# Performance work log

Measured on AMD Instinct MI355X. Metric: run time of the kernel, lower is better.

The kernel has to match this reference:

```python
import jax, jax.numpy as jnp
import numpy as np

NUM_HEADS = 16
ROPE_BASE = 50.0


def _apply_rope(x):
    # x: [b, s, h, d]; torchtune-style rotary embedding with base=ROPE_BASE
    b, s, h, d = x.shape
    inv_freq = 1.0 / (ROPE_BASE ** (jnp.arange(0, d, 2, dtype=jnp.float32) / d))  # [d/2]
    angles = jnp.arange(s, dtype=jnp.float32)[:, None] * inv_freq[None, :]         # [s, d/2]
    cos = jnp.cos(angles)[None, :, None, :]  # [1, s, 1, d/2]
    sin = jnp.sin(angles)[None, :, None, :]
    xr = x.reshape(b, s, h, d // 2, 2)
    x0, x1 = xr[..., 0], xr[..., 1]
    out = jnp.stack([x0 * cos - x1 * sin, x1 * cos + x0 * sin], axis=-1)
    return out.reshape(b, s, h, d).astype(x.dtype)


def setup_inputs() -> dict:
    key = jax.random.key(0)
    k1, k2, k3 = jax.random.split(key, 3)
    B, S, D = 2, 2048, 1024
    x = jax.random.normal(k1, (B, S, D), dtype=jnp.float32)
    w_qkv = jax.random.normal(k2, (3 * D, D), dtype=jnp.float32) * (D ** -0.5)
    w_out = jax.random.normal(k3, (D, D), dtype=jnp.float32) * (D ** -0.5)
    b_out = jnp.zeros((D,), dtype=jnp.float32)
    return {"x": x, "w_qkv": w_qkv, "w_out": w_out, "b_out": b_out}


def reference(x, w_qkv, w_out, b_out):
    B, S, D = x.shape
    H = NUM_HEADS
    dk = D // H

    qkv = x @ w_qkv.T                       # [b, s, 3D]
    q, k, v = jnp.split(qkv, 3, axis=-1)
    q = q.reshape(B, S, H, dk)
    k = k.reshape(B, S, H, dk)
    q = _apply_rope(q)
    k = _apply_rope(k)
    q = q.transpose(0, 2, 1, 3)             # [b, h, s, d]
    k = k.transpose(0, 2, 1, 3)
    v = v.reshape(B, S, H, dk).transpose(0, 2, 1, 3)

    scale = 1.0 / jnp.sqrt(jnp.asarray(dk, dtype=x.dtype))
    scores = jnp.einsum('bhsd,bhtd->bhst', q, k) * scale  # [b, h, s, s]
    # additive diagonal mask: -inf on the diagonal (blocks self-attention)
    eye = jnp.eye(S, dtype=bool)
    scores = jnp.where(eye[None, None], -jnp.inf, scores)
    attn = jax.nn.softmax(scores, axis=-1)
    out = jnp.einsum('bhst,bhtd->bhsd', attn, v)          # [b, h, s, d]
    out = out.transpose(0, 2, 1, 3).reshape(B, S, D)
    return out @ w_out.T + b_out
```

## Files before the change

kernel.cpp:

```cpp
#include <hip/hip_runtime.h>
#include <hip/hip_bf16.h>
#include <math.h>

#define D_MODEL 1024
#define NHEADS  16
#define DK      64
#define SEQ     2048
#define BATCH   2
#define QTILE   128

typedef __attribute__((ext_vector_type(8)))  short  short8;
typedef __attribute__((ext_vector_type(8)))  unsigned short ushort8;
typedef __attribute__((ext_vector_type(4)))  float  floatx4;
typedef __attribute__((ext_vector_type(16))) float  floatx16;

__device__ __forceinline__ unsigned short f2bf(float f) {
    union { float f; unsigned int u; } v; v.f = f;
    unsigned int u = v.u;
    return (unsigned short)((u + 0x7FFFu + ((u >> 16) & 1u)) >> 16);
}
__device__ __forceinline__ float bf2f(unsigned short u) {
    union { unsigned int u; float f; } v; v.u = ((unsigned int)u) << 16;
    return v.f;
}
__device__ __forceinline__ unsigned int fau(float f) {
    union { float f; unsigned int u; } v; v.f = f; return v.u;
}

__device__ __forceinline__ void gload_lds16(const unsigned short* g, unsigned short* l) {
    __builtin_amdgcn_global_load_lds((__attribute__((address_space(1))) const void*)g,
                                     (__attribute__((address_space(3))) void*)l,
                                     16, 0, 0);
}

#define X8 ((BATCH * SEQ * D_MODEL) / 8)
#define W8 ((3 * D_MODEL * D_MODEL) / 8)
#define O8 ((D_MODEL * D_MODEL) / 8)
__global__ __launch_bounds__(256) void pack_all(const float* __restrict__ x,
                                                const float* __restrict__ wq,
                                                const float* __restrict__ wo,
                                                unsigned short* __restrict__ xb,
                                                unsigned short* __restrict__ wqb,
                                                unsigned short* __restrict__ wob) {
    const int t = blockIdx.x * blockDim.x + threadIdx.x;
    const float* src; unsigned short* dst; int idx;
    if (t < X8)           { src = x;  dst = xb;  idx = t; }
    else if (t < X8 + W8) { src = wq; dst = wqb; idx = t - X8; }
    else if (t < X8 + W8 + O8) { src = wo; dst = wob; idx = t - X8 - W8; }
    else return;
    const float4 a = ((const float4*)src)[2 * idx];
    const float4 b = ((const float4*)src)[2 * idx + 1];
    short8 o;
    o[0] = (short)f2bf(a.x); o[1] = (short)f2bf(a.y);
    o[2] = (short)f2bf(a.z); o[3] = (short)f2bf(a.w);
    o[4] = (short)f2bf(b.x); o[5] = (short)f2bf(b.y);
    o[6] = (short)f2bf(b.z); o[7] = (short)f2bf(b.w);
    ((short8*)dst)[idx] = o;
}

template <int TM, typename OUT_T>
__global__ __launch_bounds__(256) void gemm_bf16(const unsigned short* __restrict__ A,
                                                 const unsigned short* __restrict__ B,
                                                 const float* __restrict__ bias,
                                                 OUT_T* __restrict__ C,
                                                 int M, int N, int K) {
    constexpr int NAF = TM / 32;
    __shared__ __align__(16) unsigned short As[TM][32];
    __shared__ __align__(16) unsigned short Bs[128][32];

    const int tid  = threadIdx.x;
    const int wave = tid >> 6;
    const int lane = tid & 63;
    const int quad = lane >> 4;
    const int lcol = lane & 15;
    const int wr   = (wave >> 1) * (TM / 2);
    const int wc   = (wave & 1) * 64;
    const int tm   = blockIdx.y * TM;
    const int tn   = blockIdx.x * 128;

    const int srowA = wave * (TM / 4) + (lane >> 2);
    const int srowB = wave * 32 + (lane >> 2);
    const int scol  = (lane & 3) * 8;
    const unsigned short* gB0 = B + (size_t)(tn + srowB) * K + scol;
    const unsigned short* gB1 = gB0 + (size_t)16 * K;
    unsigned short* lB0 = &Bs[wave * 32][0];
    unsigned short* lB1 = &Bs[wave * 32 + 16][0];

    floatx4 acc[NAF][4];
#pragma unroll
    for (int i = 0; i < NAF; ++i)
#pragma unroll
        for (int j = 0; j < 4; ++j) acc[i][j] = (floatx4){0.f, 0.f, 0.f, 0.f};

    for (int k0 = 0; k0 < K; k0 += 32) {
        __syncthreads();
#pragma unroll
        for (int u = 0; u < TM / 64; ++u)
            gload_lds16(A + (size_t)(tm + srowA + u * 16) * K + k0 + scol,
                        &As[wave * (TM / 4) + u * 16][0]);
        gload_lds16(gB0 + k0, lB0);
        gload_lds16(gB1 + k0, lB1);
        __syncthreads();

        short8 af[NAF], bf[4];
#pragma unroll
        for (int i = 0; i < NAF; ++i) af[i] = *(short8*)&As[wr + i * 16 + lcol][quad * 8];
#pragma unroll
        for (int j = 0; j < 4; ++j) bf[j] = *(short8*)&Bs[wc + j * 16 + lcol][quad * 8];
#pragma unroll
        for (int i = 0; i < NAF; ++i)
#pragma unroll
            for (int j = 0; j < 4; ++j)
                acc[i][j] = __builtin_amdgcn_mfma_f32_16x16x32_bf16(af[i], bf[j], acc[i][j], 0, 0, 0);
    }

#pragma unroll
    for (int i = 0; i < NAF; ++i) {
#pragma unroll
        for (int r = 0; r < 4; ++r) {
            const int row = tm + wr + i * 16 + quad * 4 + r;
#pragma unroll
            for (int j = 0; j < 4; ++j) {
                const int col = tn + wc + j * 16 + lcol;
                float v = acc[i][j][r];
                if (bias) v += bias[col];
                if constexpr (sizeof(OUT_T) == 2)
                    C[(size_t)row * N + col] = (OUT_T)f2bf(v);
                else
                    C[(size_t)row * N + col] = (OUT_T)v;
            }
        }
    }
}

__global__ __launch_bounds__(256) void rope_vtrans(const unsigned short* __restrict__ qkvb,
                                                   unsigned short* __restrict__ Qb,
                                                   unsigned short* __restrict__ Kb,
                                                   unsigned short* __restrict__ Vtg) {
    const int st = blockIdx.x, h = blockIdx.y, b = blockIdx.z;
    const int tid = threadIdx.x;
    const int s0 = st * 64;

    const int i  = tid & 31;
    const int r0 = tid >> 5;
    const float inv_freq = exp2f(-(2.0f * (float)i / (float)DK) * log2f(50.0f));
    const float QSCALE = 0.125f * 1.44269504f;
#pragma unroll
    for (int pass = 0; pass < 8; ++pass) {
        const int s = s0 + r0 + pass * 8;
        const size_t in_base = ((size_t)(b * SEQ + s)) * (3 * D_MODEL) + h * DK + 2 * i;
        const float q0 = bf2f(qkvb[in_base]),           q1 = bf2f(qkvb[in_base + 1]);
        const float k0 = bf2f(qkvb[in_base + D_MODEL]), k1 = bf2f(qkvb[in_base + D_MODEL + 1]);
        float sn, cs;
        __sincosf((float)s * inv_freq, &sn, &cs);
        const size_t ob = (((size_t)(b * NHEADS + h)) * SEQ + s) * DK + 2 * i;
        const unsigned int qw = (unsigned int)f2bf((q0 * cs - q1 * sn) * QSCALE)
                              | ((unsigned int)f2bf((q1 * cs + q0 * sn) * QSCALE) << 16);
        const unsigned int kw = (unsigned int)f2bf(k0 * cs - k1 * sn)
                              | ((unsigned int)f2bf(k1 * cs + k0 * sn) << 16);
        *(unsigned int*)&Qb[ob] = qw;
        *(unsigned int*)&Kb[ob] = kw;
    }

    __shared__ unsigned short Lt[64][65];
    const int r = tid >> 3;
    const int c = (tid & 7) * 8;
    const size_t in_row = ((size_t)(b * SEQ + s0 + r)) * (3 * D_MODEL) + 2 * D_MODEL + h * DK + c;
    const ushort8 v0 = *(const ushort8*)&qkvb[in_row];
    const ushort8 v1 = *(const ushort8*)&qkvb[in_row + (size_t)32 * (3 * D_MODEL)];
    const int u0 = r, u1 = r + 32;
    const int kc0 = (u0 & 48) | (8 * ((u0 >> 2) & 1) + (u0 & 3) + 4 * ((u0 >> 3) & 1));
    const int kc1 = (u1 & 48) | (8 * ((u1 >> 2) & 1) + (u1 & 3) + 4 * ((u1 >> 3) & 1));
#pragma unroll
    for (int j = 0; j < 8; ++j) Lt[c + j][kc0] = v0[j];
#pragma unroll
    for (int j = 0; j < 8; ++j) Lt[c + j][kc1] = v1[j];
    __syncthreads();
    const size_t bh = (size_t)(b * NHEADS + h);
    ushort8 o0, o1;
#pragma unroll
    for (int j = 0; j < 8; ++j) { o0[j] = Lt[r][c + j]; o1[j] = Lt[r + 32][c + j]; }
    unsigned short* orow = Vtg + (bh * DK + r) * SEQ + s0 + c;
    *(ushort8*)orow = o0;
    *(ushort8*)(orow + (size_t)32 * SEQ) = o1;
}

#define LDW 72

__global__ __launch_bounds__(512, 4) void flash_attn(const unsigned short* __restrict__ Qb,
                                                     const unsigned short* __restrict__ Kb,
                                                     const unsigned short* __restrict__ Vtg,
                                                     unsigned short* __restrict__ attnb) {
    const int tid  = threadIdx.x;
    const int wave = tid >> 6;
    const int lane = tid & 63;
    const int l31  = lane & 31;
    const int lh   = lane >> 5;
    const int mh2  = wave & 3;
    const int kh   = wave >> 2;
    const int kb   = kh * 32;

    const int f  = blockIdx.x + gridDim.x * (blockIdx.y + gridDim.y * blockIdx.z);
    const int w  = (f & 7) * 64 + (f >> 3);
    const int qt = w & 15;
    const int h  = (w >> 4) & 15;
    const int b  = w >> 8;

    __shared__ __align__(16) unsigned char smem[36864];
    unsigned short (*Ks0)[LDW] = (unsigned short (*)[LDW])(smem);
    unsigned short (*Vt0)[LDW] = (unsigned short (*)[LDW])(smem +  9216);
    unsigned short (*Ks1)[LDW] = (unsigned short (*)[LDW])(smem + 18432);
    unsigned short (*Vt1)[LDW] = (unsigned short (*)[LDW])(smem + 27648);
    float (*Ored)[68] = (float (*)[68])smem;
    float* lred0 = (float*)(smem + 34816);
    float* lred1 = lred0 + 128;

    const size_t bh = (size_t)(b * NHEADS + h);
    const unsigned short* Qg = Qb + (bh * SEQ + (size_t)qt * QTILE) * DK;
    const unsigned short* Kg = Kb + bh * SEQ * DK;
    const unsigned short* Vg = Vtg + bh * (size_t)DK * SEQ;

    short8 qf[4];
#pragma unroll
    for (int t = 0; t < 4; ++t)
        qf[t] = *(const short8*)&Qg[(size_t)(mh2 * 32 + l31) * DK + t * 16 + lh * 8];

    const int strow = tid >> 3;
    const int stcol = (tid & 7) * 8;
    const unsigned short* kg = &Kg[(size_t)strow * DK + stcol];
    const unsigned short* vg = &Vg[(size_t)strow * SEQ + stcol];

    short8 kr = *(const short8*)&kg[0];
    short8 vr = *(const short8*)&vg[0];

    floatx16 oacc[2];
    oacc[0] = (floatx16)(0.f);
    oacc[1] = (floatx16)(0.f);
    float lp = 0.f;

    const int diagkt = qt * QTILE + mh2 * 32 - kb;

    auto compute = [&](unsigned short (*Ks)[LDW], unsigned short (*Vt)[LDW], int kt) {
        floatx16 sc = (floatx16)(0.f);
        __builtin_amdgcn_s_setprio(1);
#pragma unroll
        for (int t = 0; t < 4; ++t) {
            const short8 kf = *(short8*)&Ks[kb + l31][t * 16 + lh * 8];
            sc = __builtin_amdgcn_mfma_f32_32x32x16_bf16(kf, qf[t], sc, 0, 0, 0);
        }
        __builtin_amdgcn_s_setprio(0);

        if (kt == diagkt) {
#pragma unroll
            for (int r = 0; r < 16; ++r) {
                const int key_loc = (r & 3) + 8 * (r >> 2) + 4 * lh;
                if (key_loc == l31) sc[r] = -1e30f;
            }
        }

        short8 pf0, pf1;
        {
            union { unsigned int u[4]; short8 s8; } a, c;
#pragma unroll
            for (int d = 0; d < 4; ++d) {
                const float e0 = __builtin_amdgcn_exp2f(sc[2 * d]);
                const float e1 = __builtin_amdgcn_exp2f(sc[2 * d + 1]);
                a.u[d] = __builtin_amdgcn_perm(fau(e1), fau(e0), 0x07060302u);
                const float f0 = __builtin_amdgcn_exp2f(sc[8 + 2 * d]);
                const float f1 = __builtin_amdgcn_exp2f(sc[8 + 2 * d + 1]);
                c.u[d] = __builtin_amdgcn_perm(fau(f1), fau(f0), 0x07060302u);
                lp += (e0 + e1) + (f0 + f1);
            }
            pf0 = a.s8;
            pf1 = c.s8;
        }

        __builtin_amdgcn_s_setprio(1);
#pragma unroll
        for (int nd = 0; nd < 2; ++nd) {
            const short8 vfa = *(short8*)&Vt[nd * 32 + l31][kb + lh * 8];
            const short8 vfb = *(short8*)&Vt[nd * 32 + l31][kb + 16 + lh * 8];
            oacc[nd] = __builtin_amdgcn_mfma_f32_32x32x16_bf16(pf0, vfa, oacc[nd], 0, 0, 0);
            oacc[nd] = __builtin_amdgcn_mfma_f32_32x32x16_bf16(pf1, vfb, oacc[nd], 0, 0, 0);
        }
        __builtin_amdgcn_s_setprio(0);
    };

    for (int kt = 0; kt < SEQ; kt += 128) {
        *(short8*)&Ks0[strow][stcol] = kr;
        *(short8*)&Vt0[strow][stcol] = vr;
        __syncthreads();
        kr = *(const short8*)&kg[(size_t)(kt + 64) * DK];
        vr = *(const short8*)&vg[kt + 64];
        compute(Ks0, Vt0, kt);

        *(short8*)&Ks1[strow][stcol] = kr;
        *(short8*)&Vt1[strow][stcol] = vr;
        __syncthreads();
        const int ktn = (kt + 128 < SEQ) ? kt + 128 : 0;
        kr = *(const short8*)&kg[(size_t)ktn * DK];
        vr = *(const short8*)&vg[ktn];
        compute(Ks1, Vt1, kt + 64);
    }

    const float lptot = lp + __shfl_xor(lp, 32, 64);

    __syncthreads();
    if (lh == 0) {
        if (kh == 0) lred0[mh2 * 32 + l31] = lptot;
        else         lred1[mh2 * 32 + l31] = lptot;
    }
    if (kh == 1) {
#pragma unroll
        for (int r = 0; r < 16; ++r) {
            const int m = mh2 * 32 + (r & 3) + 8 * (r >> 2) + 4 * lh;
            Ored[m][l31]      = oacc[0][r];
            Ored[m][32 + l31] = oacc[1][r];
        }
    }
    __syncthreads();
    if (kh == 0) {
        unsigned short* obase = attnb + ((size_t)b * SEQ + (size_t)qt * QTILE) * D_MODEL + h * DK;
#pragma unroll
        for (int r = 0; r < 16; ++r) {
            const int m = mh2 * 32 + (r & 3) + 8 * (r >> 2) + 4 * lh;
            const float inv = 1.001953125f / (lred0[m] + lred1[m]);
            const float v0 = (oacc[0][r] + Ored[m][l31]) * inv;
            const float v1 = (oacc[1][r] + Ored[m][32 + l31]) * inv;
            obase[(size_t)m * D_MODEL + l31]      = f2bf(v0);
            obase[(size_t)m * D_MODEL + 32 + l31] = f2bf(v1);
        }
    }
}

extern "C" void kernel_launch(void* const* d_in, const int* in_sizes, int n_in,
                              void* d_out, int out_size, void* d_ws, size_t ws_size,
                              hipStream_t stream) {
    const float* x     = (const float*)d_in[0];
    const float* w_qkv = (const float*)d_in[1];
    const float* w_out = (const float*)d_in[2];
    const float* b_out = (const float*)d_in[3];
    float* out = (float*)d_out;

    const int M = BATCH * SEQ;
    const size_t X_ELEMS    = (size_t)M * D_MODEL;
    const size_t WQKV_ELEMS = (size_t)3 * D_MODEL * D_MODEL;
    const size_t WOUT_ELEMS = (size_t)D_MODEL * D_MODEL;
    const size_t QKV_ELEMS  = (size_t)M * 3 * D_MODEL;
    const size_t HEAD_ELEMS = (size_t)BATCH * NHEADS * SEQ * DK;

    unsigned short* xb    = (unsigned short*)d_ws;
    unsigned short* wqkvb = xb + X_ELEMS;
    unsigned short* woutb = wqkvb + WQKV_ELEMS;
    unsigned short* qkvb  = woutb + WOUT_ELEMS;
    unsigned short* Qb    = qkvb + QKV_ELEMS;
    unsigned short* Kb    = Qb + HEAD_ELEMS;
    unsigned short* Vtg   = Kb + HEAD_ELEMS;
    unsigned short* attnb = Vtg + HEAD_ELEMS;

    pack_all<<<(X8 + W8 + O8 + 255) / 256, 256, 0, stream>>>(x, w_qkv, w_out, xb, wqkvb, woutb);

    {
        dim3 grid(3 * D_MODEL / 128, M / 128);
        gemm_bf16<128, unsigned short><<<grid, 256, 0, stream>>>(xb, wqkvb, nullptr, qkvb,
                                                                 M, 3 * D_MODEL, D_MODEL);
    }
    {
        dim3 grid(SEQ / 64, NHEADS, BATCH);
        rope_vtrans<<<grid, 256, 0, stream>>>(qkvb, Qb, Kb, Vtg);
    }
    {
        dim3 grid(SEQ / QTILE, NHEADS, BATCH);
        flash_attn<<<grid, 512, 0, stream>>>(Qb, Kb, Vtg, attnb);
    }
    {
        dim3 grid(D_MODEL / 128, M / 64);
        gemm_bf16<64, float><<<grid, 256, 0, stream>>>(attnb, woutb, b_out, out,
                                                       M, D_MODEL, D_MODEL);
    }
}
```

Before: 195.2 us.

## Replace QKV GEMM with 256x256-tile, 8-wave, four-phase pipelined kernel

Adds a dedicated QKV projection GEMM that uses 256x256 output tiles, 512 threads, double-buffered LDS with XOR-swizzled direct global-to-LDS loads, and splits each K step into four quadrant phases that interleave staging of the next tile with MFMA work. Blocks are remapped so that groups of consecutive block IDs are spread across rows of the output. The aim is more reuse per loaded byte and better overlap of memory with compute than the generic 128x128 kernel. The large tile gives only 192 blocks and raises register and LDS pressure, which may hurt occupancy. The final iteration also issues a redundant prefetch of k-tile 0.

```diff
diff --git a/kernel.cpp b/kernel.cpp
--- a/kernel.cpp
+++ b/kernel.cpp
@@ -1,6 +1,7 @@
 #include <hip/hip_runtime.h>
 #include <hip/hip_bf16.h>
 #include <math.h>
+#include <type_traits>
 
 #define D_MODEL 1024
 #define NHEADS  16
@@ -133,6 +134,121 @@
     }
 }
 
+#define QKV_M 4096
+#define QKV_N 3072
+#define QKV_K 1024
+#define QKV_NT (QKV_K / 64)
+
+__global__ __launch_bounds__(512, 2) void gemm_qkv_8ph(const unsigned short* __restrict__ A,
+                                                        const unsigned short* __restrict__ B,
+                                                        unsigned short* __restrict__ C) {
+    __shared__ __align__(16) unsigned short As[2][256][64];
+    __shared__ __align__(16) unsigned short Bs[2][256][64];
+
+    const int tid  = threadIdx.x;
+    const int w    = tid >> 6;
+    const int lane = tid & 63;
+    const int quad = lane >> 4;
+    const int lcol = lane & 15;
+    const int wr   = w >> 2;
+    const int wc   = w & 3;
+
+    const int f  = blockIdx.x;
+    const int wg = (f & 7) * 24 + (f >> 3);
+    const int tn = (wg % (QKV_N / 256)) * 256;
+    const int tm = (wg / (QKV_N / 256)) * 256;
+
+    const int srow8 = lane >> 3;
+    const int sj    = lane & 7;
+
+    auto stageA = [&](int buf, int kt, int mh) {
+#pragma unroll
+        for (int c = 0; c < 2; ++c) {
+            const int r0 = mh * 64 + c * 128 + w * 8;
+            const int r  = r0 + srow8;
+            gload_lds16(A + (size_t)(tm + r) * QKV_K + kt * 64 + ((sj ^ (r & 7)) * 8),
+                        &As[buf][r0][0]);
+        }
+    };
+    auto stageB = [&](int buf, int kt, int nh) {
+#pragma unroll
+        for (int c = 0; c < 2; ++c) {
+            const int rho0 = c * 64 + w * 8;
+            const int r0   = (rho0 >> 5) * 64 + nh * 32 + (rho0 & 31);
+            const int r    = r0 + srow8;
+            gload_lds16(B + (size_t)(tn + r) * QKV_K + kt * 64 + ((sj ^ (r & 7)) * 8),
+                        &Bs[buf][r0][0]);
+        }
+    };
+
+    floatx4 acc[8][4];
+#pragma unroll
+    for (int i = 0; i < 8; ++i)
+#pragma unroll
+        for (int j = 0; j < 4; ++j) acc[i][j] = (floatx4){0.f, 0.f, 0.f, 0.f};
+
+    auto do_phase = [&](int buf, auto mhc, auto nhc, auto stager) {
+        constexpr int mh = decltype(mhc)::value;
+        constexpr int nh = decltype(nhc)::value;
+        asm volatile("s_waitcnt vmcnt(4)" ::: "memory");
+        __builtin_amdgcn_s_barrier();
+        asm volatile("" ::: "memory");
+        short8 a[4][2], bfr[2][2];
+#pragma unroll
+        for (int i = 0; i < 4; ++i)
+#pragma unroll
+            for (int kk = 0; kk < 2; ++kk) {
+                const int r = wr * 128 + mh * 64 + i * 16 + lcol;
+                a[i][kk] = *(const short8*)&As[buf][r][((kk * 4 + quad) ^ (r & 7)) * 8];
+            }
+#pragma unroll
+        for (int j = 0; j < 2; ++j)
+#pragma unroll
+            for (int kk = 0; kk < 2; ++kk) {
+                const int r = wc * 64 + nh * 32 + j * 16 + lcol;
+                bfr[j][kk] = *(const short8*)&Bs[buf][r][((kk * 4 + quad) ^ (r & 7)) * 8];
+            }
+        stager();
+        __builtin_amdgcn_s_setprio(1);
+#pragma unroll
+        for (int i = 0; i < 4; ++i)
+#pragma unroll
+            for (int j = 0; j < 2; ++j)
+#pragma unroll
+                for (int kk = 0; kk < 2; ++kk)
+                    acc[mh * 4 + i][nh * 2 + j] = __builtin_amdgcn_mfma_f32_16x16x32_bf16(
+                        a[i][kk], bfr[j][kk], acc[mh * 4 + i][nh * 2 + j], 0, 0, 0);
+        __builtin_amdgcn_s_setprio(0);
+    };
+
+    using IC0 = std::integral_constant<int, 0>;
+    using IC1 = std::integral_constant<int, 1>;
+
+    stageA(0, 0, 0); stageB(0, 0, 0); stageB(0, 0, 1); stageA(0, 0, 1);
+
+    for (int t = 0; t < QKV_NT; ++t) {
+        const int buf = t & 1, nb = buf ^ 1;
+        const int kn = (t + 1 == QKV_NT) ? 0 : t + 1;
+        do_phase(buf, IC0{}, IC0{}, [&] { stageA(nb, kn, 0); });
+        do_phase(buf, IC0{}, IC1{}, [&] { stageB(nb, kn, 0); });
+        do_phase(buf, IC1{}, IC0{}, [&] { stageB(nb, kn, 1); });
+        do_phase(buf, IC1{}, IC1{}, [&] { stageA(nb, kn, 1); });
+    }
+
+#pragma unroll
+    for (int i = 0; i < 8; ++i) {
+#pragma unroll
+        for (int rr = 0; rr < 4; ++rr) {
+            const int row = tm + wr * 128 + i * 16 + quad * 4 + rr;
+#pragma unroll
+            for (int jf = 0; jf < 4; ++jf) {
+                const int col = tn + wc * 64 + jf * 16 + lcol;
+                C[(size_t)row * QKV_N + col] = f2bf(acc[i][jf][rr]);
+            }
+        }
+    }
+}
+
 __global__ __launch_bounds__(256) void rope_vtrans(const unsigned short* __restrict__ qkvb,
                                                    unsigned short* __restrict__ Qb,
                                                    unsigned short* __restrict__ Kb,
@@ -360,11 +476,8 @@
 
     pack_all<<<(X8 + W8 + O8 + 255) / 256, 256, 0, stream>>>(x, w_qkv, w_out, xb, wqkvb, woutb);
 
-    {
-        dim3 grid(3 * D_MODEL / 128, M / 128);
-        gemm_bf16<128, unsigned short><<<grid, 256, 0, stream>>>(xb, wqkvb, nullptr, qkvb,
-                                                                 M, 3 * D_MODEL, D_MODEL);
-    }
+    gemm_qkv_8ph<<<(QKV_M / 256) * (QKV_N / 256), 512, 0, stream>>>(xb, wqkvb, qkvb);
+
     {
         dim3 grid(SEQ / 64, NHEADS, BATCH);
         rope_vtrans<<<grid, 256, 0, stream>>>(qkvb, Qb, Kb, Vtg);
```

Result: faster. 186.7 us (-4.4%).
